# Kernel optimization log

Measured on AMD Instinct MI355X. Metric: run time of the kernel, lower is better.

## Reference

```python
import jax, jax.numpy as jnp
import numpy as np

B, S, H = 2, 1024, 2048          # batch, seq, hidden
E, K = 8, 2                       # num experts, top-k
I = 1408                          # moe_intermediate_size
IS = 5632                         # shared_expert_intermediate_size
WSCALE = 0.02


def setup_inputs() -> dict:
    key = jax.random.key(0)
    ks = jax.random.split(key, 9)
    f32 = jnp.float32
    return {
        "hidden_states": jax.random.normal(ks[0], (B, S, H), dtype=f32),
        "gate_w": jax.random.normal(ks[1], (E, H), dtype=f32) * WSCALE,          # router
        "w_gate": jax.random.normal(ks[2], (E, H, I), dtype=f32) * WSCALE,       # experts.N.gate_proj
        "w_up": jax.random.normal(ks[3], (E, H, I), dtype=f32) * WSCALE,         # experts.N.up_proj
        "w_down": jax.random.normal(ks[4], (E, I, H), dtype=f32) * WSCALE,       # experts.N.down_proj
        "sw_gate": jax.random.normal(ks[5], (H, IS), dtype=f32) * WSCALE,        # shared_expert.gate_proj
        "sw_up": jax.random.normal(ks[6], (H, IS), dtype=f32) * WSCALE,          # shared_expert.up_proj
        "sw_down": jax.random.normal(ks[7], (IS, H), dtype=f32) * WSCALE,        # shared_expert.down_proj
        "shared_gate_w": jax.random.normal(ks[8], (H, 1), dtype=f32) * WSCALE,   # shared_expert_gate
    }


def reference(hidden_states, gate_w, w_gate, w_up, w_down, sw_gate, sw_up, sw_down, shared_gate_w):
    x = hidden_states                                   # [B,S,H]
    # ---- TopKGate: softmax router -> top-k weights + indices, renormalized ----
    logits = jnp.einsum("bsh,eh->bse", x, gate_w)       # [B,S,E]
    probs = jax.nn.softmax(logits, axis=-1)
    top_w, top_i = jax.lax.top_k(probs, K)              # [B,S,K]
    top_w = top_w / jnp.sum(top_w, axis=-1, keepdims=True)
    # dense combine weights per expert: sum_k top_w * (top_i == e)  -> [B,S,E]
    onehot = jax.nn.one_hot(top_i, E, dtype=x.dtype)    # [B,S,K,E]
    combine = jnp.einsum("bsk,bske->bse", top_w, onehot)
    # ---- dense all-experts SwiGLU MLP, then mask/combine (faithful to source) ----
    g = jnp.einsum("bsh,ehi->besi", x, w_gate)          # [B,E,S,I]
    u = jnp.einsum("bsh,ehi->besi", x, w_up)
    h = jax.nn.silu(g) * u
    expert_out = jnp.einsum("besi,eih->besh", h, w_down)  # [B,E,S,H]
    moe_out = jnp.einsum("besh,bse->bsh", expert_out, combine)
    # ---- shared expert with sigmoid gate ----
    sh = jax.nn.silu(x @ sw_gate) * (x @ sw_up)         # [B,S,IS]
    shared_out = sh @ sw_down                            # [B,S,H]
    shared_gate = jax.nn.sigmoid(x @ shared_gate_w)     # [B,S,1]
    return moe_out + shared_out * shared_gate
```

## Files before the change

kernel.cpp:

```cpp
#include <hip/hip_runtime.h>
#include <hip/hip_bf16.h>
#include <stdint.h>

#define TOK   2048
#define HDIM  2048
#define IDIM  1408
#define ISDIM 5632
#define NEXP  8
#define GU_GEMM_BLOCKS 1088

typedef float  f32x4  __attribute__((ext_vector_type(4)));
typedef short  bf16x8 __attribute__((ext_vector_type(8)));

__device__ __forceinline__ unsigned short f2b(float f) {
  union { float f; uint32_t u; } v; v.f = f;
  return (unsigned short)((v.u + 0x7fffu + ((v.u >> 16) & 1u)) >> 16);
}

__device__ __forceinline__ void async16(void* lds, const void* g) {
  __builtin_amdgcn_global_load_lds(
      (const __attribute__((address_space(1))) unsigned int*)g,
      (__attribute__((address_space(3))) unsigned int*)lds, 16, 0, 0);
}

#define VWAIT_BAR(N) asm volatile("s_waitcnt vmcnt(" #N ")\n\ts_barrier" ::: "memory")
#define VBAR()       asm volatile("s_barrier" ::: "memory")

__global__ __launch_bounds__(256) void router_kernel(
    const float* __restrict__ X, const float* __restrict__ GW,
    const float* __restrict__ SGW, int* __restrict__ cnt,
    int* __restrict__ tok_e, float* __restrict__ tok_w, float* __restrict__ sg)
{
  const int tkn = blockIdx.x, t = threadIdx.x;
  const float* xr = X + (size_t)tkn * HDIM;
  float a[NEXP + 1];
  #pragma unroll
  for (int e = 0; e <= NEXP; ++e) a[e] = 0.f;
  for (int h = t; h < HDIM; h += 256) {
    const float xv = xr[h];
    #pragma unroll
    for (int e = 0; e < NEXP; ++e) a[e] += xv * GW[e * HDIM + h];
    a[NEXP] += xv * SGW[h];
  }
  #pragma unroll
  for (int off = 32; off > 0; off >>= 1) {
    #pragma unroll
    for (int e = 0; e <= NEXP; ++e) a[e] += __shfl_down(a[e], off);
  }
  __shared__ float red[4][NEXP + 1];
  if ((t & 63) == 0) {
    #pragma unroll
    for (int e = 0; e <= NEXP; ++e) red[t >> 6][e] = a[e];
  }
  __syncthreads();
  if (t == 0) {
    float l[NEXP + 1];
    #pragma unroll
    for (int e = 0; e <= NEXP; ++e) l[e] = red[0][e] + red[1][e] + red[2][e] + red[3][e];
    int i1 = 0;
    #pragma unroll
    for (int e = 1; e < NEXP; ++e) if (l[e] > l[i1]) i1 = e;
    int i2 = (i1 == 0) ? 1 : 0;
    #pragma unroll
    for (int e = 0; e < NEXP; ++e) if (e != i1 && e != i2 && l[e] > l[i2]) i2 = e;
    const float w1 = 1.f / (1.f + __expf(l[i2] - l[i1]));
    tok_e[tkn * 2 + 0] = i1; tok_e[tkn * 2 + 1] = i2;
    tok_w[tkn * 2 + 0] = w1; tok_w[tkn * 2 + 1] = 1.f - w1;
    atomicAdd(&cnt[i1], 1); atomicAdd(&cnt[i2], 1);
    sg[tkn] = 1.f / (1.f + __expf(-l[NEXP]));
  }
}

__global__ void scan_kernel(const int* __restrict__ cnt, int* __restrict__ offs) {
  if (threadIdx.x == 0) {
    int r = 0;
    for (int e = 0; e < NEXP; ++e) { offs[e] = r; r += cnt[e]; }
  }
}

__global__ __launch_bounds__(256) void build_kernel(
    const int* __restrict__ tok_e, const float* __restrict__ tok_w,
    const int* __restrict__ offs, int* __restrict__ cur,
    int* __restrict__ list, float* __restrict__ wl)
{
  const int tkn = blockIdx.x * 256 + threadIdx.x;
  if (tkn >= TOK) return;
  #pragma unroll
  for (int k = 0; k < 2; ++k) {
    const int e = tok_e[tkn * 2 + k];
    const int pos = atomicAdd(&cur[e], 1);
    const int slot = offs[e] + pos;
    list[slot] = tkn;
    wl[slot] = tok_w[tkn * 2 + k];
  }
}

__global__ __launch_bounds__(256) void cvt_kernel(
    const float* __restrict__ src, unsigned short* __restrict__ dst, int n4)
{
  const int i = blockIdx.x * 512 + threadIdx.x;
  #pragma unroll
  for (int p = 0; p < 2; ++p) {
    const int j = i + p * 256;
    if (j < n4) {
      const float4 v = ((const float4*)src)[j];
      ushort4 b; b.x = f2b(v.x); b.y = f2b(v.y); b.z = f2b(v.z); b.w = f2b(v.w);
      ((ushort4*)dst)[j] = b;
    }
  }
}

__global__ __launch_bounds__(256) void transpose_cvt_kernel(
    const float* __restrict__ src, unsigned short* __restrict__ dst,
    const int R, const int C)
{
  __shared__ unsigned short tile[64][72];
  const size_t mat = (size_t)blockIdx.z * R * C;
  const int c0 = blockIdx.x * 64, r0 = blockIdx.y * 64;
  const int t = threadIdx.x;
  const int rr = t >> 4, cc = (t & 15) * 4;
  #pragma unroll
  for (int p = 0; p < 4; ++p) {
    const int r = rr + p * 16;
    const float4 v = *(const float4*)(src + mat + (size_t)(r0 + r) * C + c0 + cc);
    tile[cc + 0][r] = f2b(v.x);
    tile[cc + 1][r] = f2b(v.y);
    tile[cc + 2][r] = f2b(v.z);
    tile[cc + 3][r] = f2b(v.w);
  }
  __syncthreads();
  #pragma unroll
  for (int p = 0; p < 2; ++p) {
    const int id = p * 256 + t;
    const int c = id >> 3, q = id & 7;
    const uint4 v = *(const uint4*)&tile[c][q * 8];
    *(uint4*)(dst + mat + (size_t)(c0 + c) * R + r0 + q * 8) = v;
  }
}

__global__ __launch_bounds__(512) void gateup_fused_kernel(
    const unsigned short* __restrict__ Xb,
    const unsigned short* __restrict__ Wshg, const unsigned short* __restrict__ Wshu,
    const unsigned short* __restrict__ Wexg, const unsigned short* __restrict__ Wexu,
    unsigned short* __restrict__ shb, unsigned short* __restrict__ hb,
    const int* __restrict__ list, const int* __restrict__ offs, const int* __restrict__ cnt,
    const float* __restrict__ swDown, const float* __restrict__ wDown,
    unsigned short* __restrict__ W5, unsigned short* __restrict__ W6)
{
  __shared__ char smem[65536];
  const int t = threadIdx.x;

  if (blockIdx.x >= GU_GEMM_BLOCKS) {
    const int half = t >> 8;
    const int t2 = t & 255;
    int tid2 = (blockIdx.x - GU_GEMM_BLOCKS) * 2 + half;
    const float* src; unsigned short* dst; int R, cx, ry;
    if (tid2 < 2816) {
      src = swDown; dst = W5; R = ISDIM; cx = tid2 & 31; ry = tid2 >> 5;
    } else {
      tid2 -= 2816;
      const int e = tid2 / 704, rem = tid2 % 704;
      cx = rem & 31; ry = rem >> 5;
      src = wDown + (size_t)e * IDIM * HDIM;
      dst = W6 + (size_t)e * HDIM * IDIM;
      R = IDIM;
    }
    unsigned short (*tile)[72] = (unsigned short(*)[72])(smem + half * 16384);
    const int c0 = cx * 64, r0 = ry * 64;
    const int rr = t2 >> 4, cc = (t2 & 15) * 4;
    #pragma unroll
    for (int p = 0; p < 4; ++p) {
      const int r = rr + p * 16;
      const float4 v = *(const float4*)(src + (size_t)(r0 + r) * HDIM + c0 + cc);
      tile[cc + 0][r] = f2b(v.x);
      tile[cc + 1][r] = f2b(v.y);
      tile[cc + 2][r] = f2b(v.z);
      tile[cc + 3][r] = f2b(v.w);
    }
    __syncthreads();
    #pragma unroll
    for (int p = 0; p < 2; ++p) {
      const int id = p * 256 + t2;
      const int ci = id >> 3, q = id & 7;
      *(uint4*)(dst + (size_t)(c0 + ci) * R + r0 + q * 8) = *(const uint4*)&tile[ci][q * 8];
    }
    return;
  }

  const int xcd = blockIdx.x & 7;
  const int local = blockIdx.x >> 3;
  const int c = xcd + 8 * (local >> 3);
  const int mt = local & 7;
  if (c >= 132) return;

  int rowbase, mcnt, n0, N, gather;
  const unsigned short *Wg, *Wu;
  unsigned short* Cout;
  if (c < 44) {
    N = ISDIM; n0 = c * 128; rowbase = mt * 256; mcnt = 256; gather = 0;
    Wg = Wshg; Wu = Wshu; Cout = shb;
  } else {
    const int cE = c - 44;
    const int e = cE / 11, n = cE % 11;
    mcnt = cnt[e] - mt * 256;
    if (mcnt <= 0) return;
    N = IDIM; n0 = n * 128; rowbase = offs[e] + mt * 256; gather = 1;
    Wg = Wexg + (size_t)e * IDIM * HDIM;
    Wu = Wexu + (size_t)e * IDIM * HDIM;
    Cout = hb;
  }

  const int wid = t >> 6, lane = t & 63;
  const int wm = wid >> 1, wn = wid & 1;
  const int lcol = lane & 15, lk = lane >> 4;

  f32x4 accg[4][4], accu[4][4];
  #pragma unroll
  for (int i = 0; i < 4; ++i)
    #pragma unroll
    for (int j = 0; j < 4; ++j) { accg[i][j] = {0.f,0.f,0.f,0.f}; accu[i][j] = {0.f,0.f,0.f,0.f}; }

  int arow[2], akoff[2];
  #pragma unroll
  for (int p = 0; p < 2; ++p) {
    const int s = p * 512 + t;
    const int m = s >> 2;
    akoff[p] = (((s & 3) ^ ((m >> 1) & 3)) << 3);
    arow[p] = gather ? list[rowbase + m] : (rowbase + m);
  }
  const int albase0 = (t & 448) * 16;
  const int albase1 = (512 + (t & 448)) * 16;
  const int bmrow = n0 + (t >> 2);
  const int bkoff = (((t & 3) ^ (((t >> 2) >> 1) & 3)) << 3);
  const int blbase = (t & 448) * 16;

#define STAGE_GU(BUF, K0) do {                                                    \
    async16(smem + (BUF) + albase0,        Xb + (size_t)arow[0] * HDIM + (K0) + akoff[0]); \
    async16(smem + (BUF) + albase1,        Xb + (size_t)arow[1] * HDIM + (K0) + akoff[1]); \
    async16(smem + (BUF) + 16384 + blbase, Wg + (size_t)bmrow * HDIM + (K0) + bkoff); \
    async16(smem + (BUF) + 24576 + blbase, Wu + (size_t)bmrow * HDIM + (K0) + bkoff); \
  } while (0)

#define COMPUTE_GU(BUF) do {                                                      \
    bf16x8 af[4], bg[4], bu[4];                                                   \
    _Pragma("unroll")                                                             \
    for (int fm = 0; fm < 4; ++fm) {                                              \
      const int m = wm * 64 + fm * 16 + lcol;                                     \
      af[fm] = *(const bf16x8*)(smem + (BUF) + m * 64 + (((lk ^ ((m >> 1) & 3)) & 3) << 4)); \
    }                                                                             \
    _Pragma("unroll")                                                             \
    for (int fn = 0; fn < 4; ++fn) {                                              \
      const int n = wn * 64 + fn * 16 + lcol;                                     \
      const int ra = n * 64 + (((lk ^ ((n >> 1) & 3)) & 3) << 4);                 \
      bg[fn] = *(const bf16x8*)(smem + (BUF) + 16384 + ra);                       \
      bu[fn] = *(const bf16x8*)(smem + (BUF) + 24576 + ra);                       \
    }                                                                             \
    _Pragma("unroll")                                                             \
    for (int fm = 0; fm < 4; ++fm)                                                \
      _Pragma("unroll")                                                           \
      for (int fn = 0; fn < 4; ++fn) {                                            \
        accg[fm][fn] = __builtin_amdgcn_mfma_f32_16x16x32_bf16(af[fm], bg[fn], accg[fm][fn], 0, 0, 0); \
        accu[fm][fn] = __builtin_amdgcn_mfma_f32_16x16x32_bf16(af[fm], bu[fn], accu[fm][fn], 0, 0, 0); \
      } } while (0)

  STAGE_GU(0, 0);
  for (int it = 0; it < 31; ++it) {
    STAGE_GU(32768, (2 * it + 1) * 32);
    VWAIT_BAR(4);
    COMPUTE_GU(0);
    VBAR();
    STAGE_GU(0, (2 * it + 2) * 32);
    VWAIT_BAR(4);
    COMPUTE_GU(32768);
    VBAR();
  }
  STAGE_GU(32768, 63 * 32);
  VWAIT_BAR(4);
  COMPUTE_GU(0);
  VBAR();
  VWAIT_BAR(0);
  COMPUTE_GU(32768);
#undef STAGE_GU
#undef COMPUTE_GU

  #pragma unroll
  for (int fm = 0; fm < 4; ++fm) {
    #pragma unroll
    for (int fn = 0; fn < 4; ++fn) {
      const int col = n0 + wn * 64 + fn * 16 + lcol;
      #pragma unroll
      for (int r = 0; r < 4; ++r) {
        const int lrow = wm * 64 + fm * 16 + lk * 4 + r;
        if (lrow < mcnt) {
          const float gv = accg[fm][fn][r];
          const float uv = accu[fm][fn][r];
          const float hv = gv * uv / (1.f + __expf(-gv));
          Cout[(size_t)(rowbase + lrow) * N + col] = f2b(hv);
        }
      }
    }
  }
}

__global__ __launch_bounds__(512) void down_fused_kernel(
    const unsigned short* __restrict__ shb, const unsigned short* __restrict__ hb,
    const unsigned short* __restrict__ WdshT, const unsigned short* __restrict__ WdexT,
    float* __restrict__ out,
    const int* __restrict__ list, const float* __restrict__ wl, const float* __restrict__ sg,
    const int* __restrict__ offs, const int* __restrict__ cnt)
{
  __shared__ char smem[49152];

  const int xcd = blockIdx.x & 7;
  const int local = blockIdx.x >> 3;
  const int c = xcd + 8 * (local >> 3);
  const int mt = local & 7;
  const int t = threadIdx.x;

  int rowbase, mcnt, n0, K, kbeg, em;
  const unsigned short *Ap, *Bp;
  if (c < 64) {
    const int pn = c & 15, ksp = c >> 4;
    rowbase = mt * 256; mcnt = 256; n0 = pn * 128;
    K = ISDIM; kbeg = ksp * 44; em = 0;
    Ap = shb; Bp = WdshT;
  } else {
    const int cE = c - 64;
    const int e = cE >> 4, n = cE & 15;
    mcnt = cnt[e] - mt * 256;
    if (mcnt <= 0) return;
    rowbase = offs[e] + mt * 256; n0 = n * 128;
    K = IDIM; kbeg = 0; em = 1;
    Ap = hb; Bp = WdexT + (size_t)e * HDIM * IDIM;
  }

  const int wid = t >> 6, lane = t & 63;
  const int wm = wid >> 1, wn = wid & 1;
  const int lcol = lane & 15, lk = lane >> 4;

  f32x4 acc[4][4];
  #pragma unroll
  for (int i = 0; i < 4; ++i)
    #pragma unroll
    for (int j = 0; j < 4; ++j) acc[i][j] = {0.f,0.f,0.f,0.f};

  int amrow[2], akoff[2];
  #pragma unroll
  for (int p = 0; p < 2; ++p) {
    const int s = p * 512 + t;
    const int m = s >> 2;
    akoff[p] = (((s & 3) ^ ((m >> 1) & 3)) << 3);
    int rw = rowbase + m;
    if (em && rw > 4223) rw = 4223;
    amrow[p] = rw;
  }
  const int albase0 = (t & 448) * 16;
  const int albase1 = (512 + (t & 448)) * 16;
  const int bmrow = n0 + (t >> 2);
  const int bkoff = (((t & 3) ^ (((t >> 2) >> 1) & 3)) << 3);
  const int blbase = (t & 448) * 16;

#define STAGE_D(BUF, K0) do {                                                     \
    async16(smem + (BUF) + albase0,        Ap + (size_t)amrow[0] * K + (K0) + akoff[0]); \
    async16(smem + (BUF) + albase1,        Ap + (size_t)amrow[1] * K + (K0) + akoff[1]); \
    async16(smem + (BUF) + 16384 + blbase, Bp + (size_t)bmrow * K + (K0) + bkoff); \
  } while (0)

#define COMPUTE_D(BUF) do {                                                       \
    bf16x8 af[4], bfr[4];                                                         \
    _Pragma("unroll")                                                             \
    for (int fm = 0; fm < 4; ++fm) {                                              \
      const int m = wm * 64 + fm * 16 + lcol;                                     \
      af[fm] = *(const bf16x8*)(smem + (BUF) + m * 64 + (((lk ^ ((m >> 1) & 3)) & 3) << 4)); \
    }                                                                             \
    _Pragma("unroll")                                                             \
    for (int fn = 0; fn < 4; ++fn) {                                              \
      const int n = wn * 64 + fn * 16 + lcol;                                     \
      bfr[fn] = *(const bf16x8*)(smem + (BUF) + 16384 + n * 64 + (((lk ^ ((n >> 1) & 3)) & 3) << 4)); \
    }                                                                             \
    _Pragma("unroll")                                                             \
    for (int fm = 0; fm < 4; ++fm)                                                \
      _Pragma("unroll")                                                           \
      for (int fn = 0; fn < 4; ++fn)                                              \
        acc[fm][fn] = __builtin_amdgcn_mfma_f32_16x16x32_bf16(af[fm], bfr[fn], acc[fm][fn], 0, 0, 0); \
  } while (0)

  const int kb = kbeg * 32;
  STAGE_D(0, kb);
  for (int it = 0; it < 21; ++it) {
    STAGE_D(24576, kb + (2 * it + 1) * 32);
    VWAIT_BAR(3);
    COMPUTE_D(0);
    VBAR();
    STAGE_D(0, kb + (2 * it + 2) * 32);
    VWAIT_BAR(3);
    COMPUTE_D(24576);
    VBAR();
  }
  STAGE_D(24576, kb + 43 * 32);
  VWAIT_BAR(3);
  COMPUTE_D(0);
  VBAR();
  VWAIT_BAR(0);
  COMPUTE_D(24576);
#undef STAGE_D
#undef COMPUTE_D

  #pragma unroll
  for (int fm = 0; fm < 4; ++fm) {
    #pragma unroll
    for (int fn = 0; fn < 4; ++fn) {
      const int col = n0 + wn * 64 + fn * 16 + lcol;
      #pragma unroll
      for (int r = 0; r < 4; ++r) {
        const int lrow = wm * 64 + fm * 16 + lk * 4 + r;
        if (lrow < mcnt) {
          const float v = acc[fm][fn][r];
          const int sl = rowbase + lrow;
          const int orow = em ? list[sl] : sl;
          const float sc = em ? wl[sl] : sg[sl];
          atomicAdd(out + (size_t)orow * HDIM + col, sc * v);
        }
      }
    }
  }
}

extern "C" void kernel_launch(void* const* d_in, const int* in_sizes, int n_in,
                              void* d_out, int out_size, void* d_ws, size_t ws_size,
                              hipStream_t stream)
{
  const float* x       = (const float*)d_in[0];
  const float* gate_w  = (const float*)d_in[1];
  const float* w_gate  = (const float*)d_in[2];
  const float* w_up    = (const float*)d_in[3];
  const float* w_down  = (const float*)d_in[4];
  const float* sw_gate = (const float*)d_in[5];
  const float* sw_up   = (const float*)d_in[6];
  const float* sw_down = (const float*)d_in[7];
  const float* sgw     = (const float*)d_in[8];

  float* out = (float*)d_out;
  char* ws = (char*)d_ws;

  const size_t NEED_OVL   = 251100000;
  const size_t NEED_FUSED = 182000000;

  if (ws_size >= NEED_OVL) {
    unsigned short* Xb  = (unsigned short*)ws;
    unsigned short* W1  = (unsigned short*)(ws + 8388608);
    unsigned short* W2  = (unsigned short*)(ws + 31457280);
    unsigned short* W3  = (unsigned short*)(ws + 54525952);
    unsigned short* W4  = (unsigned short*)(ws + 100663296);
    unsigned short* W5  = (unsigned short*)(ws + 146800640);
    unsigned short* W6  = (unsigned short*)(ws + 169869312);
    unsigned short* shb = (unsigned short*)(ws + 216006656);
    unsigned short* hb  = (unsigned short*)(ws + 239075328);
    char* meta = ws + 250970112;
    int*   cnt   = (int*)(meta);
    int*   cur   = (int*)(meta + 256);
    int*   offs  = (int*)(meta + 512);
    int*   list  = (int*)(meta + 768);
    float* wl    = (float*)(meta + 768 + 18432);
    int*   tok_e = (int*)(meta + 768 + 2 * 18432);
    float* tok_w = (float*)(meta + 768 + 2 * 18432 + 16384);
    float* sg    = (float*)(meta + 768 + 2 * 18432 + 32768);

    hipMemsetAsync(meta, 0, 768 + 2 * 18432, stream);
    hipMemsetAsync(out, 0, (size_t)TOK * HDIM * 4, stream);

    cvt_kernel<<<TOK * HDIM / 4 / 512, 256, 0, stream>>>(x, Xb, TOK * HDIM / 4);
    router_kernel<<<TOK, 256, 0, stream>>>(x, gate_w, sgw, cnt, tok_e, tok_w, sg);
    scan_kernel<<<1, 64, 0, stream>>>(cnt, offs);
    build_kernel<<<8, 256, 0, stream>>>(tok_e, tok_w, offs, cur, list, wl);

    transpose_cvt_kernel<<<dim3(ISDIM / 64, HDIM / 64, 1), 256, 0, stream>>>(sw_gate, W1, HDIM, ISDIM);
    transpose_cvt_kernel<<<dim3(ISDIM / 64, HDIM / 64, 1), 256, 0, stream>>>(sw_up,   W2, HDIM, ISDIM);
    transpose_cvt_kernel<<<dim3(IDIM / 64, HDIM / 64, NEXP), 256, 0, stream>>>(w_gate, W3, HDIM, IDIM);
    transpose_cvt_kernel<<<dim3(IDIM / 64, HDIM / 64, NEXP), 256, 0, stream>>>(w_up,   W4, HDIM, IDIM);

    gateup_fused_kernel<<<GU_GEMM_BLOCKS + 4224, 512, 0, stream>>>(
        Xb, W1, W2, W3, W4, shb, hb, list, offs, cnt, sw_down, w_down, W5, W6);

    down_fused_kernel<<<1536, 512, 0, stream>>>(shb, hb, W5, W6, out, list, wl, sg, offs, cnt);
  } else if (ws_size >= NEED_FUSED) {
    unsigned short* Xb  = (unsigned short*)ws;
    unsigned short* W1  = (unsigned short*)(ws + 8388608);
    unsigned short* W2  = (unsigned short*)(ws + 31457280);
    unsigned short* W3  = (unsigned short*)(ws + 54525952);
    unsigned short* W4  = (unsigned short*)(ws + 100663296);
    unsigned short* shb = (unsigned short*)(ws + 146800640);
    unsigned short* hb  = (unsigned short*)(ws + 169869312);
    char* meta = ws + 181764096;
    int*   cnt   = (int*)(meta);
    int*   cur   = (int*)(meta + 256);
    int*   offs  = (int*)(meta + 512);
    int*   list  = (int*)(meta + 768);
    float* wl    = (float*)(meta + 768 + 18432);
    int*   tok_e = (int*)(meta + 768 + 2 * 18432);
    float* tok_w = (float*)(meta + 768 + 2 * 18432 + 16384);
    float* sg    = (float*)(meta + 768 + 2 * 18432 + 32768);

    hipMemsetAsync(meta, 0, 768 + 2 * 18432, stream);
    hipMemsetAsync(out, 0, (size_t)TOK * HDIM * 4, stream);

    cvt_kernel<<<TOK * HDIM / 4 / 512, 256, 0, stream>>>(x, Xb, TOK * HDIM / 4);
    router_kernel<<<TOK, 256, 0, stream>>>(x, gate_w, sgw, cnt, tok_e, tok_w, sg);
    scan_kernel<<<1, 64, 0, stream>>>(cnt, offs);
    build_kernel<<<8, 256, 0, stream>>>(tok_e, tok_w, offs, cur, list, wl);

    transpose_cvt_kernel<<<dim3(ISDIM / 64, HDIM / 64, 1), 256, 0, stream>>>(sw_gate, W1, HDIM, ISDIM);
    transpose_cvt_kernel<<<dim3(ISDIM / 64, HDIM / 64, 1), 256, 0, stream>>>(sw_up,   W2, HDIM, ISDIM);
    transpose_cvt_kernel<<<dim3(IDIM / 64, HDIM / 64, NEXP), 256, 0, stream>>>(w_gate, W3, HDIM, IDIM);
    transpose_cvt_kernel<<<dim3(IDIM / 64, HDIM / 64, NEXP), 256, 0, stream>>>(w_up,   W4, HDIM, IDIM);

    gateup_fused_kernel<<<GU_GEMM_BLOCKS, 512, 0, stream>>>(
        Xb, W1, W2, W3, W4, shb, hb, list, offs, cnt, nullptr, nullptr, nullptr, nullptr);

    transpose_cvt_kernel<<<dim3(HDIM / 64, ISDIM / 64, 1), 256, 0, stream>>>(sw_down, W1, ISDIM, HDIM);
    transpose_cvt_kernel<<<dim3(HDIM / 64, IDIM / 64, NEXP), 256, 0, stream>>>(w_down, W3, IDIM, HDIM);

    down_fused_kernel<<<1536, 512, 0, stream>>>(shb, hb, W1, W3, out, list, wl, sg, offs, cnt);
  }
}
```

Baseline: 587.4 us.

## Merge gate/up weight transposes into one launch and interleave down-transpose blocks with GEMM

Replaces four separate transpose-convert launches for the gate/up weights with a single kernel that dispatches over all four matrices by block index. In the fused gate-up GEMM kernel, the down-projection transpose blocks are now interleaved with GEMM blocks (one GEMM block per five), instead of all being appended after the GEMM blocks. The intent is to cut launch overhead and let the memory-bound transpose work run alongside the compute-bound GEMM tiles rather than trailing them. Because GEMM block indices now depend on b/5, the XCD-aware mapping changes, which could affect cache locality.

```diff
diff --git a/kernel.cpp b/kernel.cpp
--- a/kernel.cpp
+++ b/kernel.cpp
@@ -7,7 +7,6 @@
 #define IDIM  1408
 #define ISDIM 5632
 #define NEXP  8
-#define GU_GEMM_BLOCKS 1088
 
 typedef float  f32x4  __attribute__((ext_vector_type(4)));
 typedef short  bf16x8 __attribute__((ext_vector_type(8)));
@@ -138,6 +137,47 @@
   }
 }
 
+__global__ __launch_bounds__(256) void transpose_gu_kernel(
+    const float* __restrict__ sw_gate, const float* __restrict__ sw_up,
+    const float* __restrict__ w_gate,  const float* __restrict__ w_up,
+    unsigned short* __restrict__ W1, unsigned short* __restrict__ W2,
+    unsigned short* __restrict__ W3, unsigned short* __restrict__ W4)
+{
+  __shared__ unsigned short tile[64][72];
+  int b = blockIdx.x;
+  const float* src; unsigned short* dst;
+  int srcC, dstLen, cx, ry;
+  if (b < 2816)       { src = sw_gate; dst = W1; srcC = ISDIM; dstLen = HDIM; cx = b % 88; ry = b / 88; }
+  else if (b < 5632)  { b -= 2816; src = sw_up; dst = W2; srcC = ISDIM; dstLen = HDIM; cx = b % 88; ry = b / 88; }
+  else if (b < 11264) { b -= 5632; const int e = b / 704, r = b % 704;
+                        src = w_gate + (size_t)e * HDIM * IDIM; dst = W3 + (size_t)e * IDIM * HDIM;
+                        srcC = IDIM; dstLen = HDIM; cx = r % 22; ry = r / 22; }
+  else                { b -= 11264; const int e = b / 704, r = b % 704;
+                        src = w_up + (size_t)e * HDIM * IDIM; dst = W4 + (size_t)e * IDIM * HDIM;
+                        srcC = IDIM; dstLen = HDIM; cx = r % 22; ry = r / 22; }
+
+  const int c0 = cx * 64, r0 = ry * 64;
+  const int t = threadIdx.x;
+  const int rr = t >> 4, cc = (t & 15) * 4;
+  #pragma unroll
+  for (int p = 0; p < 4; ++p) {
+    const int r = rr + p * 16;
+    const float4 v = *(const float4*)(src + (size_t)(r0 + r) * srcC + c0 + cc);
+    tile[cc + 0][r] = f2b(v.x);
+    tile[cc + 1][r] = f2b(v.y);
+    tile[cc + 2][r] = f2b(v.z);
+    tile[cc + 3][r] = f2b(v.w);
+  }
+  __syncthreads();
+  #pragma unroll
+  for (int p = 0; p < 2; ++p) {
+    const int id = p * 256 + t;
+    const int ci = id >> 3, q = id & 7;
+    *(uint4*)(dst + (size_t)(c0 + ci) * dstLen + r0 + q * 8) = *(const uint4*)&tile[ci][q * 8];
+  }
+}
+
+template<int MODE>
 __global__ __launch_bounds__(512) void gateup_fused_kernel(
     const unsigned short* __restrict__ Xb,
     const unsigned short* __restrict__ Wshg, const unsigned short* __restrict__ Wshu,
@@ -149,46 +189,55 @@
 {
   __shared__ char smem[65536];
   const int t = threadIdx.x;
-
-  if (blockIdx.x >= GU_GEMM_BLOCKS) {
-    const int half = t >> 8;
-    const int t2 = t & 255;
-    int tid2 = (blockIdx.x - GU_GEMM_BLOCKS) * 2 + half;
-    const float* src; unsigned short* dst; int R, cx, ry;
-    if (tid2 < 2816) {
-      src = swDown; dst = W5; R = ISDIM; cx = tid2 & 31; ry = tid2 >> 5;
-    } else {
-      tid2 -= 2816;
-      const int e = tid2 / 704, rem = tid2 % 704;
-      cx = rem & 31; ry = rem >> 5;
-      src = wDown + (size_t)e * IDIM * HDIM;
-      dst = W6 + (size_t)e * HDIM * IDIM;
-      R = IDIM;
+  int gidx;
+
+  if (MODE == 1) {
+    const int b = blockIdx.x;
+    if (b % 5 != 0) {
+      const int tix = b - (b / 5 + 1);
+      if (tix >= 4224) return;
+      const int half = t >> 8;
+      const int t2 = t & 255;
+      int tid2 = tix * 2 + half;
+      const float* src; unsigned short* dst; int R, cx, ry;
+      if (tid2 < 2816) {
+        src = swDown; dst = W5; R = ISDIM; cx = tid2 & 31; ry = tid2 >> 5;
+      } else {
+        tid2 -= 2816;
+        const int e = tid2 / 704, rem = tid2 % 704;
+        cx = rem & 31; ry = rem >> 5;
+        src = wDown + (size_t)e * IDIM * HDIM;
+        dst = W6 + (size_t)e * HDIM * IDIM;
+        R = IDIM;
+      }
+      unsigned short (*tile)[72] = (unsigned short(*)[72])(smem + half * 16384);
+      const int c0 = cx * 64, r0 = ry * 64;
+      const int rr = t2 >> 4, cc = (t2 & 15) * 4;
+      #pragma unroll
+      for (int p = 0; p < 4; ++p) {
+        const int r = rr + p * 16;
+        const float4 v = *(const float4*)(src + (size_t)(r0 + r) * HDIM + c0 + cc);
+        tile[cc + 0][r] = f2b(v.x);
+        tile[cc + 1][r] = f2b(v.y);
+        tile[cc + 2][r] = f2b(v.z);
+        tile[cc + 3][r] = f2b(v.w);
+      }
+      __syncthreads();
+      #pragma unroll
+      for (int p = 0; p < 2; ++p) {
+        const int id = p * 256 + t2;
+        const int ci = id >> 3, q = id & 7;
+        *(uint4*)(dst + (size_t)(c0 + ci) * R + r0 + q * 8) = *(const uint4*)&tile[ci][q * 8];
+      }
+      return;
     }
-    unsigned short (*tile)[72] = (unsigned short(*)[72])(smem + half * 16384);
-    const int c0 = cx * 64, r0 = ry * 64;
-    const int rr = t2 >> 4, cc = (t2 & 15) * 4;
-    #pragma unroll
-    for (int p = 0; p < 4; ++p) {
-      const int r = rr + p * 16;
-      const float4 v = *(const float4*)(src + (size_t)(r0 + r) * HDIM + c0 + cc);
-      tile[cc + 0][r] = f2b(v.x);
-      tile[cc + 1][r] = f2b(v.y);
-      tile[cc + 2][r] = f2b(v.z);
-      tile[cc + 3][r] = f2b(v.w);
-    }
-    __syncthreads();
-    #pragma unroll
-    for (int p = 0; p < 2; ++p) {
-      const int id = p * 256 + t2;
-      const int ci = id >> 3, q = id & 7;
-      *(uint4*)(dst + (size_t)(c0 + ci) * R + r0 + q * 8) = *(const uint4*)&tile[ci][q * 8];
-    }
-    return;
-  }
-
-  const int xcd = blockIdx.x & 7;
-  const int local = blockIdx.x >> 3;
+    gidx = b / 5;
+  } else {
+    gidx = blockIdx.x;
+  }
+
+  const int xcd = gidx & 7;
+  const int local = gidx >> 3;
   const int c = xcd + 8 * (local >> 3);
   const int mt = local & 7;
   if (c >= 132) return;
@@ -474,12 +523,10 @@
     scan_kernel<<<1, 64, 0, stream>>>(cnt, offs);
     build_kernel<<<8, 256, 0, stream>>>(tok_e, tok_w, offs, cur, list, wl);
 
-    transpose_cvt_kernel<<<dim3(ISDIM / 64, HDIM / 64, 1), 256, 0, stream>>>(sw_gate, W1, HDIM, ISDIM);
-    transpose_cvt_kernel<<<dim3(ISDIM / 64, HDIM / 64, 1), 256, 0, stream>>>(sw_up,   W2, HDIM, ISDIM);
-    transpose_cvt_kernel<<<dim3(IDIM / 64, HDIM / 64, NEXP), 256, 0, stream>>>(w_gate, W3, HDIM, IDIM);
-    transpose_cvt_kernel<<<dim3(IDIM / 64, HDIM / 64, NEXP), 256, 0, stream>>>(w_up,   W4, HDIM, IDIM);
-
-    gateup_fused_kernel<<<GU_GEMM_BLOCKS + 4224, 512, 0, stream>>>(
+    transpose_gu_kernel<<<16896, 256, 0, stream>>>(
+        sw_gate, sw_up, w_gate, w_up, W1, W2, W3, W4);
+
+    gateup_fused_kernel<1><<<5436, 512, 0, stream>>>(
         Xb, W1, W2, W3, W4, shb, hb, list, offs, cnt, sw_down, w_down, W5, W6);
 
     down_fused_kernel<<<1536, 512, 0, stream>>>(shb, hb, W5, W6, out, list, wl, sg, offs, cnt);
@@ -514,7 +561,7 @@
     transpose_cvt_kernel<<<dim3(IDIM / 64, HDIM / 64, NEXP), 256, 0, stream>>>(w_gate, W3, HDIM, IDIM);
     transpose_cvt_kernel<<<dim3(IDIM / 64, HDIM / 64, NEXP), 256, 0, stream>>>(w_up,   W4, HDIM, IDIM);
 
-    gateup_fused_kernel<<<GU_GEMM_BLOCKS, 512, 0, stream>>>(
+    gateup_fused_kernel<0><<<1088, 512, 0, stream>>>(
         Xb, W1, W2, W3, W4, shb, hb, list, offs, cnt, nullptr, nullptr, nullptr, nullptr);
 
     transpose_cvt_kernel<<<dim3(HDIM / 64, ISDIM / 64, 1), 256, 0, stream>>>(sw_down, W1, ISDIM, HDIM);
```

After: 602.8 us. 2.6% more time.
